# Kernel tuning notes

Hardware: AMD Instinct MI355X
Metric: run time of the kernel (lower is better)

The kernel has to match this reference:

```python
import jax, jax.numpy as jnp
import numpy as np

B, S, D, H, F, E = 2, 1024, 1024, 16, 2048, 8
HD = D // H


def _ln(x, g, b, eps=1e-5):
    m = x.mean(-1, keepdims=True)
    v = ((x - m) ** 2).mean(-1, keepdims=True)
    return (x - m) / jnp.sqrt(v + eps) * g + b


def setup_inputs() -> dict:
    key = jax.random.key(0)
    ks = jax.random.split(key, 12)
    rn = lambda k, shp, s=0.02: jax.random.normal(k, shp, jnp.float32) * s
    return {
        'src': jax.random.normal(ks[0], (B, S, D), jnp.float32),
        'q_w': rn(ks[1], (D, D)),
        'k_w': rn(ks[2], (D, D)),
        'v_w': rn(ks[3], (D, D)),
        'out_w': rn(ks[4], (D, D)),
        'gate_w': rn(ks[5], (D, D)),
        'gate_b': rn(ks[6], (D,)),
        'scale_w': rn(ks[7], (H, HD)),
        'n1_g': jnp.ones((D,), jnp.float32),
        'n1_b': jnp.zeros((D,), jnp.float32),
        'n2_g': jnp.ones((D,), jnp.float32),
        'n2_b': jnp.zeros((D,), jnp.float32),
        'moe_gate_w': rn(ks[8], (D, E)),
        'moe_gate_b': jnp.zeros((E,), jnp.float32),
        'w1': rn(ks[9], (E, D, F)),
        'b1': jnp.zeros((E, F), jnp.float32),
        'ln_g': jnp.ones((E, F), jnp.float32),
        'ln_b': jnp.zeros((E, F), jnp.float32),
        'w2': rn(ks[10], (E, F, D)),
        'b2': jnp.zeros((E, D), jnp.float32),
        'res_scale': jnp.ones((E,), jnp.float32),
    }


def reference(src, q_w, k_w, v_w, out_w, gate_w, gate_b, scale_w,
              n1_g, n1_b, n2_g, n2_b, moe_gate_w, moe_gate_b,
              w1, b1, ln_g, ln_b, w2, b2, res_scale):
    b, s, d = src.shape
    h = scale_w.shape[0]
    hd = d // h
    # --- MemoAttention (gated, dynamically scaled), eval mode ---
    q = (src @ q_w).reshape(b, s, h, hd).transpose(0, 2, 1, 3)  # [b,h,s,hd]
    k = (src @ k_w).reshape(b, s, h, hd).transpose(0, 2, 1, 3)
    v = (src @ v_w).reshape(b, s, h, hd).transpose(0, 2, 1, 3)
    scores = jnp.einsum('bhqd,bhkd->bhqk', q, k) / np.float32(np.sqrt(hd))
    scale = jax.nn.sigmoid(jnp.einsum('bhsd,hd->bhs', q, scale_w)) * 2.0
    scores = scores * scale[..., None]
    aw = jax.nn.softmax(scores, axis=-1)
    out = jnp.einsum('bhqk,bhkd->bhqd', aw, v).transpose(0, 2, 1, 3).reshape(b, s, d)
    gate = jax.nn.sigmoid(out @ gate_w + gate_b)
    attn = (out * gate) @ out_w
    # --- residual + norm1 ---
    x = _ln(src + attn, n1_g, n1_b)
    # --- MoE FFN (top-2 routing; torch loop overwrites -> last (max-index) expert
    xr = x.reshape(-1, d)                      # [N, d]
    n = xr.shape[0]
    logits = xr @ moe_gate_w + moe_gate_b       # [N, E]
    top_v, top_i = jax.lax.top_k(logits, 2)
    wts = jax.nn.softmax(top_v, axis=-1)        # [N, 2]
    chosen = jnp.max(top_i, axis=-1)            # last-written expert per token

    def expert(W1, B1, G, Bt, W2, B2, rsc):
        hh = xr @ W1 + B1                       # [N, F]
        hh = jax.nn.gelu(_ln(hh, G, Bt), approximate=False)
        return (hh @ W2 + B2) * rsc + xr        # [N, d]

    outs = jax.vmap(expert)(w1, b1, ln_g, ln_b, w2, b2, res_scale)  # [E,N,d]
    sel = jnp.take_along_axis(outs.transpose(1, 0, 2), chosen[:, None, None], axis=1)[:, 0]
    moe = sel * jnp.sum(wts, axis=-1, keepdims=True)
    # --- residual + norm2 ---
    return _ln(x + moe.reshape(b, s, d), n2_g, n2_b)
```

## Files before the change

### kernel.cpp

```cpp
#include <hip/hip_runtime.h>


typedef _Float16 f16;
typedef _Float16 f16x8 __attribute__((ext_vector_type(8)));
typedef _Float16 f16x4 __attribute__((ext_vector_type(4)));
typedef float f32x4 __attribute__((ext_vector_type(4)));

constexpr int CS  = 1024;
constexpr int CD  = 1024;
constexpr int CH  = 16;
constexpr int CHD = 64;
constexpr int CF  = 2048;
constexpr int CE  = 8;
constexpr int CN  = 2048;
constexpr int CBH = 32;
constexpr int KS  = 512;
constexpr int MAXT = 48;

constexpr float LO_SCALE = 2048.f;
constexpr float LO_INV   = 1.f / 2048.f;

#define MFMA16(a, b, c) __builtin_amdgcn_mfma_f32_16x16x32_f16((a), (b), (c), 0, 0, 0)

#define TO_GBL(p) ((const __attribute__((address_space(1))) void*)(p))
#define TO_LDS(p) ((__attribute__((address_space(3))) void*)(p))
#define GLD16(g, l) __builtin_amdgcn_global_load_lds(TO_GBL(g), TO_LDS(l), 16, 0, 0)

__device__ __forceinline__ void fsplit(float v, f16 &hi, f16 &lo) {
  hi = (f16)v;
  lo = (f16)((v - (float)hi) * LO_SCALE);
}


__global__ void k_split_cvt(const float* __restrict__ in, f16* __restrict__ oh,
                            f16* __restrict__ ol, int n) {
  int i = (blockIdx.x * blockDim.x + threadIdx.x) * 4;
  if (i >= n) return;
  float4 v = *(const float4*)(in + i);
  float a[4] = {v.x, v.y, v.z, v.w};
  f16x4 vh, vl;
#pragma unroll
  for (int j = 0; j < 4; ++j) {
    f16 hi = (f16)a[j];
    vh[j] = hi;
    vl[j] = (f16)((a[j] - (float)hi) * LO_SCALE);
  }
  *(f16x4*)(oh + i) = vh;
  *(f16x4*)(ol + i) = vl;
}

// ... 2 lines not shown
    f16* __restrict__ ol, int R, int C) {
  __shared__ float t[64][65];
  const int z = blockIdx.z;
  const float* src = in + (size_t)z * R * C;
  f16* dh = oh + (size_t)z * R * C;
  f16* dl = ol ? ol + (size_t)z * R * C : nullptr;
  const int c0 = blockIdx.x * 64, r0 = blockIdx.y * 64;
  const int tt = threadIdx.x;
  const int lane = tt & 63, wv = tt >> 6;
#pragma unroll
  for (int i = 0; i < 16; ++i)
    t[wv + i * 4][lane] = src[(size_t)(r0 + wv + i * 4) * C + c0 + lane];
  __syncthreads();
  const int oc = tt >> 4;
  const int og = tt & 15;
#pragma unroll
  for (int cc = 0; cc < 64; cc += 16) {
    f16x4 vh, vl;
#pragma unroll
    for (int j = 0; j < 4; ++j) {
      const float v = t[og * 4 + j][cc + oc];
      f16 hi = (f16)v;
      vh[j] = hi;
      vl[j] = (f16)((v - (float)hi) * LO_SCALE);
    }
    const size_t idx = (size_t)(c0 + cc + oc) * R + r0 + og * 4;
    *(f16x4*)(dh + idx) = vh;
    if (dl) *(f16x4*)(dl + idx) = vl;
  }
}


template <bool SPLIT>
__device__ __forceinline__ void gemm_tile_db(
    const f16* aH, const f16* aL, const f16* bH, const f16* bL,
    size_t bRowStride , int K, f16* lds,
    f32x4 (&accm)[2][4], f32x4 (&accc)[2][4]) {
  constexpr int BUF = SPLIT ? 12288 : 6144;
  constexpr int BOFF = SPLIT ? 4096 : 2048;
  const int t = threadIdx.x;
  const int lane = t & 63, wave = t >> 6;
  const int wm = wave >> 1, wn = wave & 1;
  const int m16 = lane & 15, quad = lane >> 4;
  int aoff[2], boff[4];
#pragma unroll
  for (int sm = 0; sm < 2; ++sm) {
    const int r = wm * 32 + sm * 16 + m16;
    aoff[sm] = r * 32 + ((quad ^ ((r >> 1) & 3)) * 8);
  }
#pragma unroll
  for (int sn = 0; sn < 4; ++sn) {
    const int r = wn * 64 + sn * 16 + m16;
    boff[sn] = BOFF + r * 32 + ((quad ^ ((r >> 1) & 3)) * 8);
  }
  auto stage = [&](f16* buf) {
    GLD16(aH, buf + t * 8);
    GLD16(bH, buf + BOFF + t * 8);
    GLD16(bH + bRowStride, buf + BOFF + 2048 + t * 8);
    if constexpr (SPLIT) {
      GLD16(aL, buf + 2048 + t * 8);
      GLD16(bL, buf + 8192 + t * 8);
      GLD16(bL + bRowStride, buf + 10240 + t * 8);
      aL += 32; bL += 32;
    }
    aH += 32; bH += 32;
  };
  stage(lds);
  stage(lds + BUF);
  int cur = 0;
  for (int k = 0; k < K; k += 32) {
    if (k + 32 < K) {
      if constexpr (SPLIT) asm volatile("s_waitcnt vmcnt(6)" ::: "memory");
      else                 asm volatile("s_waitcnt vmcnt(3)" ::: "memory");
    } else {
      asm volatile("s_waitcnt vmcnt(0)" ::: "memory");
    }
    __builtin_amdgcn_s_barrier();
    asm volatile("" ::: "memory");
    f16* buf = lds + cur * BUF;
    if (k + 64 < K) {
      int pf = cur + 2; if (pf >= 3) pf -= 3;
      stage(lds + pf * BUF);
    }
    f16x8 af[2], alf[2], bf[4], blf[4];
#pragma unroll
    for (int sm = 0; sm < 2; ++sm) {
      af[sm] = *(const f16x8*)(buf + aoff[sm]);
      if constexpr (SPLIT) alf[sm] = *(const f16x8*)(buf + 2048 + aoff[sm]);
    }
#pragma unroll
    for (int sn = 0; sn < 4; ++sn) {
      bf[sn] = *(const f16x8*)(buf + boff[sn]);
      if constexpr (SPLIT) blf[sn] = *(const f16x8*)(buf + 4096 + boff[sn]);
    }
#pragma unroll
    for (int sm = 0; sm < 2; ++sm)
#pragma unroll
      for (int sn = 0; sn < 4; ++sn) {
        accm[sm][sn] = MFMA16(af[sm], bf[sn], accm[sm][sn]);
        if constexpr (SPLIT) {
          accc[sm][sn] = MFMA16(af[sm], blf[sn], accc[sm][sn]);
          accc[sm][sn] = MFMA16(alf[sm], bf[sn], accc[sm][sn]);
        }
      }
    if (++cur == 3) cur = 0;
  }
}


__global__ __launch_bounds__(256) void g_qkv(
    const f16* __restrict__ srcH, const f16* __restrict__ srcL,
    const f16* __restrict__ qwH, const f16* __restrict__ qwL,
    const f16* __restrict__ kwH, const f16* __restrict__ kwL,
    const f16* __restrict__ vwH, const f16* __restrict__ vwL,
    f16* __restrict__ qHo, f16* __restrict__ qLo,
    f16* __restrict__ kHo, f16* __restrict__ kLo,
    f16* __restrict__ vTH, f16* __restrict__ vTL) {
  __shared__ f16 lds[36864];
  const int z = blockIdx.z;
  const int m0 = blockIdx.x * 64, n0 = blockIdx.y * 128;
  const int t = threadIdx.x;
  const int rowS = t >> 2;
  const int ksw = ((t & 3) ^ ((rowS >> 1) & 3)) * 8;
  const f16* BH = (z == 0) ? qwH : (z == 1) ? kwH : vwH;
  const f16* BL = (z == 0) ? qwL : (z == 1) ? kwL : vwL;
  const f32x4 VZ = {0.f, 0.f, 0.f, 0.f};
  f32x4 accm[2][4], accc[2][4];
#pragma unroll
  for (int i = 0; i < 2; ++i)
#pragma unroll
    for (int j = 0; j < 4; ++j) { accm[i][j] = VZ; accc[i][j] = VZ; }
  gemm_tile_db<true>(srcH + (size_t)(m0 + rowS) * CD + ksw,
                     srcL + (size_t)(m0 + rowS) * CD + ksw,
                     BH + (size_t)(n0 + rowS) * CD + ksw,
                     BL + (size_t)(n0 + rowS) * CD + ksw,
                     (size_t)64 * CD, CD, lds, accm, accc);
  const int lane = t & 63, wave = t >> 6;
  const int wm = wave >> 1, wn = wave & 1;
  const int m16 = lane & 15, quad = lane >> 4;
#pragma unroll
  for (int sm = 0; sm < 2; ++sm)
#pragma unroll
    for (int sn = 0; sn < 4; ++sn)
#pragma unroll
      for (int r = 0; r < 4; ++r) {
        const int row = m0 + wm * 32 + sm * 16 + quad * 4 + r;
        const int col = n0 + wn * 64 + sn * 16 + m16;
        const float v = accm[sm][sn][r] + accc[sm][sn][r] * LO_INV;
        f16 hi, lo; fsplit(v, hi, lo);
        const int bb = row >> 10, ss = row & 1023;
        const int hh = col >> 6, hd = col & 63;
        if (z == 2) {
          const size_t idx = ((size_t)((bb * CH + hh) * CHD + hd)) * CS + ss;
          vTH[idx] = hi; vTL[idx] = lo;
        } else {
          const size_t idx = ((size_t)((bb * CH + hh) * CS + ss)) * CHD + hd;
          if (z == 0) { qHo[idx] = hi; qLo[idx] = lo; }
          else        { kHo[idx] = hi; kLo[idx] = lo; }
        }
      }
}


__device__ __forceinline__ int pswz(int q, int k) {
  return q * 64 + ((((k >> 2) ^ q) & 15) << 2) + (k & 3);
}

__global__ __launch_bounds__(256) void k_fattn(
    const f16* __restrict__ qH_, const f16* __restrict__ qL_,
    const f16* __restrict__ kH_, const f16* __restrict__ kL_,
    const f16* __restrict__ vTH_, const f16* __restrict__ vTL_,
    const float* __restrict__ scale_w,
    f16* __restrict__ aoH, f16* __restrict__ aoL) {
  __shared__ f16 kvb[32768];
  __shared__ float psc[4 * 1024];
  const int bh = blockIdx.y;
  const int b = bh >> 4, h = bh & 15;
  const int t = threadIdx.x;
  const int lane = t & 63, wave = t >> 6;
// ... 20 lines not shown
  };

  const f16* qrh = qH_ + ((size_t)bh * CS + q0 + m16) * CHD + quad * 8;
  const f16* qrl = qL_ + ((size_t)bh * CS + q0 + m16) * CHD + quad * 8;
  f16x8 a0h = *(const f16x8*)(qrh);
  f16x8 a1h = *(const f16x8*)(qrh + 32);
  f16x8 a0l = *(const f16x8*)(qrl);
  f16x8 a1l = *(const f16x8*)(qrl + 32);

  stage(kvb, 0);

  float dot = 0.f;
  {
    const float* sw = scale_w + h * CHD + quad * 8;
    float4 s0 = *(const float4*)(sw);
    float4 s1 = *(const float4*)(sw + 4);
    float4 s2 = *(const float4*)(sw + 32);
    float4 s3 = *(const float4*)(sw + 36);
    float sv[16] = {s0.x, s0.y, s0.z, s0.w, s1.x, s1.y, s1.z, s1.w,
                    s2.x, s2.y, s2.z, s2.w, s3.x, s3.y, s3.z, s3.w};
#pragma unroll
    for (int j = 0; j < 8; ++j) {
      dot += ((float)a0h[j] + (float)a0l[j] * LO_INV) * sv[j];
      dot += ((float)a1h[j] + (float)a1l[j] * LO_INV) * sv[8 + j];
    }
    dot += __shfl_xor(dot, 16);
    dot += __shfl_xor(dot, 32);
  }
  const float qsv = 2.f / (1.f + __expf(-dot));
  float qsr[4];
#pragma unroll
  for (int r = 0; r < 4; ++r) qsr[r] = __shfl(qsv, quad * 4 + r) * 0.125f;

  f32x4 accm[4], accc[4];
#pragma unroll
  for (int tt = 0; tt < 4; ++tt) { accm[tt] = VZ; accc[tt] = VZ; }
  float mrun[4], lrun[4];
#pragma unroll
  for (int r = 0; r < 4; ++r) { mrun[r] = -1e30f; lrun[r] = 0.f; }

  int cur = 0;
  for (int kc = 0; kc < CS; kc += 64) {
    __syncthreads();
    const f16* kv = kvb + cur * 16384;
    if (kc + 64 < CS) stage(kvb + (cur ^ 1) * 16384, kc + 64);

    f32x4 st[4];
#pragma unroll
    for (int tt = 0; tt < 4; ++tt) {
      const int r = tt * 16 + m16;
      f16x8 b0h = ldf(kv,        r, quad);
      f16x8 b1h = ldf(kv,        r, quad + 4);
      f16x8 b0l = ldf(kv + 4096, r, quad);
      f16x8 b1l = ldf(kv + 4096, r, quad + 4);
      f32x4 am = VZ, ac = VZ;
      am = MFMA16(a0h, b0h, am); am = MFMA16(a1h, b1h, am);
      ac = MFMA16(a0h, b0l, ac); ac = MFMA16(a0l, b0h, ac);
      ac = MFMA16(a1h, b1l, ac); ac = MFMA16(a1l, b1h, ac);
#pragma unroll
      for (int r4 = 0; r4 < 4; ++r4)
        st[tt][r4] = (am[r4] + ac[r4] * LO_INV) * qsr[r4];
    }
    float alpha[4];
#pragma unroll
    for (int r = 0; r < 4; ++r) {
      float mx = fmaxf(fmaxf(st[0][r], st[1][r]), fmaxf(st[2][r], st[3][r]));
#pragma unroll
      for (int msk = 8; msk >= 1; msk >>= 1) mx = fmaxf(mx, __shfl_xor(mx, msk));
      const float mnew = fmaxf(mrun[r], mx);
      alpha[r] = __expf(mrun[r] - mnew);
      mrun[r] = mnew;
    }
    float rs[4] = {0.f, 0.f, 0.f, 0.f};
#pragma unroll
    for (int tt = 0; tt < 4; ++tt)
#pragma unroll
      for (int r = 0; r < 4; ++r) {
        const float e = __expf(st[tt][r] - mrun[r]);
        rs[r] += e;
        P[pswz(quad * 4 + r, tt * 16 + m16)] = e;
      }
#pragma unroll
    for (int r = 0; r < 4; ++r) {
#pragma unroll
      for (int msk = 8; msk >= 1; msk >>= 1) rs[r] += __shfl_xor(rs[r], msk);
      lrun[r] = lrun[r] * alpha[r] + rs[r];
#pragma unroll
      for (int tt = 0; tt < 4; ++tt) { accm[tt][r] *= alpha[r]; accc[tt][r] *= alpha[r]; }
    }
    f16x8 pah[2], pal[2];
#pragma unroll
    for (int c = 0; c < 2; ++c) {
      const int k0 = c * 32 + quad * 8;
      float4 p0 = *(const float4*)(P + pswz(m16, k0));
      float4 p1 = *(const float4*)(P + pswz(m16, k0 + 4));
      float pv[8] = {p0.x, p0.y, p0.z, p0.w, p1.x, p1.y, p1.z, p1.w};
#pragma unroll
      for (int j = 0; j < 8; ++j) {
        f16 hi = (f16)pv[j];
        pah[c][j] = hi;
        pal[c][j] = (f16)((pv[j] - (float)hi) * LO_SCALE);
      }
    }
#pragma unroll
    for (int tt = 0; tt < 4; ++tt) {
      const int r = tt * 16 + m16;
#pragma unroll
      for (int c = 0; c < 2; ++c) {
        f16x8 vbh = ldf(kv + 8192,  r, quad + 4 * c);
        f16x8 vbl = ldf(kv + 12288, r, quad + 4 * c);
        accm[tt] = MFMA16(pah[c], vbh, accm[tt]);
        accc[tt] = MFMA16(pah[c], vbl, accc[tt]);
        accc[tt] = MFMA16(pal[c], vbh, accc[tt]);
      }
    }
    cur ^= 1;
  }
#pragma unroll
  for (int tt = 0; tt < 4; ++tt)
#pragma unroll
    for (int r = 0; r < 4; ++r) {
      const int row = q0 + quad * 4 + r;
      const float v = (accm[tt][r] + accc[tt][r] * LO_INV) / lrun[r];
      f16 hi, lo; fsplit(v, hi, lo);
      const size_t idx = ((size_t)(b * CS + row)) * CD + h * CHD + tt * 16 + m16;
      aoH[idx] = hi; aoL[idx] = lo;
    }
}


__global__ __launch_bounds__(256) void g_gate(
    const f16* __restrict__ aoH, const f16* __restrict__ aoL,
    const f16* __restrict__ gwH, const f16* __restrict__ gwL,
    float* __restrict__ gpre ) {
  __shared__ f16 lds[36864];
  const int m0 = blockIdx.x * 64, n0 = blockIdx.y * 128, s = blockIdx.z;
  const int t = threadIdx.x;
  const int rowS = t >> 2;
  const int ksw = ((t & 3) ^ ((rowS >> 1) & 3)) * 8;
  const int k0 = s * KS;
  const f32x4 VZ = {0.f, 0.f, 0.f, 0.f};
  f32x4 accm[2][4], accc[2][4];
#pragma unroll
  for (int i = 0; i < 2; ++i)
#pragma unroll
    for (int j = 0; j < 4; ++j) { accm[i][j] = VZ; accc[i][j] = VZ; }
  gemm_tile_db<true>(aoH + (size_t)(m0 + rowS) * CD + k0 + ksw,
                     aoL + (size_t)(m0 + rowS) * CD + k0 + ksw,
                     gwH + (size_t)(n0 + rowS) * CD + k0 + ksw,
                     gwL + (size_t)(n0 + rowS) * CD + k0 + ksw,
                     (size_t)64 * CD, KS, lds, accm, accc);
  float* gp = gpre + (size_t)s * CN * CD;
  const int lane = t & 63, wave = t >> 6;
  const int wm = wave >> 1, wn = wave & 1;
  const int m16 = lane & 15, quad = lane >> 4;
#pragma unroll
  for (int sm = 0; sm < 2; ++sm)
#pragma unroll
    for (int sn = 0; sn < 4; ++sn)
#pragma unroll
      for (int r = 0; r < 4; ++r) {
        const int row = m0 + wm * 32 + sm * 16 + quad * 4 + r;
        const int col = n0 + wn * 64 + sn * 16 + m16;
        gp[(size_t)row * CD + col] = accm[sm][sn][r] + accc[sm][sn][r] * LO_INV;
      }
}

__global__ __launch_bounds__(256) void k_gatemul(
    const float* __restrict__ gpre, const f16* __restrict__ aoH,
    const f16* __restrict__ aoL, const float* __restrict__ gate_b,
    f16* __restrict__ gdH, f16* __restrict__ gdL) {
  const int i = (blockIdx.x * 256 + threadIdx.x) * 4;
  float4 p0 = *(const float4*)(gpre + i);
  float4 p1 = *(const float4*)(gpre + (size_t)CN * CD + i);
  float4 gb = *(const float4*)(gate_b + (i & (CD - 1)));
  f16x4 ah = *(const f16x4*)(aoH + i);
  f16x4 al = *(const f16x4*)(aoL + i);
  float pre[4] = {p0.x + p1.x + gb.x, p0.y + p1.y + gb.y,
                  p0.z + p1.z + gb.z, p0.w + p1.w + gb.w};
  f16x4 oh, ol;
#pragma unroll
  for (int j = 0; j < 4; ++j) {
    const float g = 1.f / (1.f + __expf(-pre[j]));
    const float ov = ((float)ah[j] + (float)al[j] * LO_INV) * g;
    f16 hi, lo; fsplit(ov, hi, lo);
    oh[j] = hi; ol[j] = lo;
  }
  *(f16x4*)(gdH + i) = oh;
  *(f16x4*)(gdL + i) = ol;
}

__global__ __launch_bounds__(256) void g_outp(
    const f16* __restrict__ gdH, const f16* __restrict__ gdL,
    const f16* __restrict__ owH, const f16* __restrict__ owL,
    float* __restrict__ y1p ) {
  __shared__ f16 lds[36864];
  const int m0 = blockIdx.x * 64, n0 = blockIdx.y * 128, s = blockIdx.z;
  const int t = threadIdx.x;
  const int rowS = t >> 2;
  const int ksw = ((t & 3) ^ ((rowS >> 1) & 3)) * 8;
  const int k0 = s * KS;
  const f32x4 VZ = {0.f, 0.f, 0.f, 0.f};
  f32x4 accm[2][4], accc[2][4];
#pragma unroll
  for (int i = 0; i < 2; ++i)
#pragma unroll
    for (int j = 0; j < 4; ++j) { accm[i][j] = VZ; accc[i][j] = VZ; }
  gemm_tile_db<true>(gdH + (size_t)(m0 + rowS) * CD + k0 + ksw,
                     gdL + (size_t)(m0 + rowS) * CD + k0 + ksw,
                     owH + (size_t)(n0 + rowS) * CD + k0 + ksw,
                     owL + (size_t)(n0 + rowS) * CD + k0 + ksw,
                     (size_t)64 * CD, KS, lds, accm, accc);
  float* yp = y1p + (size_t)s * CN * CD;
  const int lane = t & 63, wave = t >> 6;
  const int wm = wave >> 1, wn = wave & 1;
  const int m16 = lane & 15, quad = lane >> 4;
#pragma unroll
  for (int sm = 0; sm < 2; ++sm)
#pragma unroll
    for (int sn = 0; sn < 4; ++sn)
#pragma unroll
      for (int r = 0; r < 4; ++r) {
        const int row = m0 + wm * 32 + sm * 16 + quad * 4 + r;
        const int col = n0 + wn * 64 + sn * 16 + m16;
        yp[(size_t)row * CD + col] = accm[sm][sn][r] + accc[sm][sn][r] * LO_INV;
      }
}


__device__ __forceinline__ void block_reduce2(float &s, float &ss, float* red) {
#pragma unroll
  for (int msk = 32; msk >= 1; msk >>= 1) {
    s += __shfl_xor(s, msk);
    ss += __shfl_xor(ss, msk);
  }
  const int wave = threadIdx.x >> 6, lane = threadIdx.x & 63;
  if (lane == 0) { red[wave] = s; red[4 + wave] = ss; }
  __syncthreads();
  s = red[0] + red[1] + red[2] + red[3];
  ss = red[4] + red[5] + red[6] + red[7];
}

__global__ __launch_bounds__(256) void k_ln1(
    const float* __restrict__ y1p, const float* __restrict__ srcp,
    const float* __restrict__ g, const float* __restrict__ bb,
    float* __restrict__ x, f16* __restrict__ xH) {
  __shared__ float red[8];
  const int n = blockIdx.x;
  const int t = threadIdx.x;
  const size_t off = (size_t)n * CD + t * 4;
  float4 v0 = *(const float4*)(y1p + off);
  float4 v1 = *(const float4*)(y1p + (size_t)CN * CD + off);
  float4 v2 = *(const float4*)(srcp + off);
  float a[4] = {v0.x + v1.x + v2.x, v0.y + v1.y + v2.y,
                v0.z + v1.z + v2.z, v0.w + v1.w + v2.w};
  float s = a[0] + a[1] + a[2] + a[3];
// ... 63 lines not shown
  for (int j = 0; j < 16; ++j) {
    const int d = lane * 16 + j;
    const float xv = xr[d];
    const float* wr = gw + (size_t)d * CE;
#pragma unroll
    for (int e = 0; e < CE; ++e) acc[e] += xv * wr[e];
  }
#pragma unroll
  for (int msk = 32; msk >= 1; msk >>= 1) {
#pragma unroll
    for (int e = 0; e < CE; ++e) acc[e] += __shfl_xor(acc[e], msk);
  }
  if (lane == 0) {
    float best = -1e30f, second = -1e30f;
    int bi = 0, si = 0;
#pragma unroll
    for (int e = 0; e < CE; ++e) {
      const float L = acc[e] + gb[e];
      if (L > best) { second = best; si = bi; best = L; bi = e; }
      else if (L > second) { second = L; si = e; }
    }
    const int ch = bi > si ? bi : si;
    chosen[n] = ch;
    const int pos = atomicAdd(&counts[ch], 1);
    bucket[ch * CN + pos] = n;
  }
}

__global__ void k_plan(const int* __restrict__ counts, int* __restrict__ tiles) {
  if (threadIdx.x == 0) {
    int n = 0;
    for (int e = 0; e < CE; ++e) {
      const int c = counts[e];
      for (int m0 = 0; m0 < c; m0 += 64) { tiles[2 * n] = e; tiles[2 * n + 1] = m0; ++n; }
    }
    for (; n < MAXT; ++n) { tiles[2 * n] = -1; tiles[2 * n + 1] = 0; }
  }
}


__global__ __launch_bounds__(256) void g_moe1(
    const f16* __restrict__ xH, const f16* __restrict__ w1t,
    const int* __restrict__ counts, const int* __restrict__ bucket,
    const int* __restrict__ tiles, float* __restrict__ hbp ) {
  const int e = tiles[2 * blockIdx.x];
  if (e < 0) return;
  const int m0 = tiles[2 * blockIdx.x + 1];
  const int cnt = counts[e];
  const int s = blockIdx.z;
  __shared__ f16 lds[18432];
  const int t = threadIdx.x;
  const int rowS = t >> 2;
  const int ksw = ((t & 3) ^ ((rowS >> 1) & 3)) * 8;
  const int k0 = s * KS;
  int ra = m0 + rowS; if (ra > cnt - 1) ra = cnt - 1;
  const int tokA = bucket[e * CN + ra];
  const int n0 = blockIdx.y * 128;
  const f32x4 VZ = {0.f, 0.f, 0.f, 0.f};
  f32x4 accm[2][4], accd[2][4];
#pragma unroll
  for (int i = 0; i < 2; ++i)
#pragma unroll
    for (int j = 0; j < 4; ++j) { accm[i][j] = VZ; accd[i][j] = VZ; }
  gemm_tile_db<false>(xH + (size_t)tokA * CD + k0 + ksw, nullptr,
                      w1t + ((size_t)e * CF + n0 + rowS) * CD + k0 + ksw, nullptr,
                      (size_t)64 * CD, KS, lds, accm, accd);
  float* hp = hbp + (size_t)s * CN * CF;
  const int lane = t & 63, wave = t >> 6;
  const int wm = wave >> 1, wn = wave & 1;
  const int m16 = lane & 15, quad = lane >> 4;
#pragma unroll
  for (int sm = 0; sm < 2; ++sm)
#pragma unroll
    for (int sn = 0; sn < 4; ++sn)
#pragma unroll
      for (int r = 0; r < 4; ++r) {
        const int rr = m0 + wm * 32 + sm * 16 + quad * 4 + r;
        if (rr >= cnt) continue;
        const int tok = bucket[e * CN + rr];
        const int col = n0 + wn * 64 + sn * 16 + m16;
        hp[(size_t)tok * CF + col] = accm[sm][sn][r];
      }
}

__global__ __launch_bounds__(256) void k_lngelu(
    const float* __restrict__ hbp, const int* __restrict__ chosen,
    const float* __restrict__ b1,
    const float* __restrict__ ln_g, const float* __restrict__ ln_b,
    f16* __restrict__ h2) {
  __shared__ float red[8];
  const int n = blockIdx.x;
  const int e = chosen[n];
  const int t = threadIdx.x;
  const size_t off = (size_t)n * CF + t * 8;
  float4 v0 = *(const float4*)(hbp + off);
  float4 v1 = *(const float4*)(hbp + off + 4);
  float4 u0 = *(const float4*)(hbp + (size_t)CN * CF + off);
  float4 u1 = *(const float4*)(hbp + (size_t)CN * CF + off + 4);
  float4 b0 = *(const float4*)(b1 + (size_t)e * CF + t * 8);
  float4 b1v = *(const float4*)(b1 + (size_t)e * CF + t * 8 + 4);
  float a[8] = {v0.x + u0.x + b0.x, v0.y + u0.y + b0.y,
                v0.z + u0.z + b0.z, v0.w + u0.w + b0.w,
                v1.x + u1.x + b1v.x, v1.y + u1.y + b1v.y,
                v1.z + u1.z + b1v.z, v1.w + u1.w + b1v.w};
  float s = 0.f, ss = 0.f;
#pragma unroll
  for (int j = 0; j < 8; ++j) { s += a[j]; ss += a[j] * a[j]; }
  block_reduce2(s, ss, red);
  const float mean = s * (1.f / CF);
  const float var = ss * (1.f / CF) - mean * mean;
  const float rstd = rsqrtf(var + 1e-5f);
  const float* g = ln_g + (size_t)e * CF;
  const float* bb = ln_b + (size_t)e * CF;
#pragma unroll
  for (int j = 0; j < 8; ++j) {
    const int d = t * 8 + j;
    const float val = (a[j] - mean) * rstd * g[d] + bb[d];
    const float gl = 0.5f * val * (1.f + erff(val * 0.70710678118654752f));
    h2[(size_t)n * CF + d] = (f16)gl;
  }
}

__global__ __launch_bounds__(256) void g_moe2(
    const f16* __restrict__ h2, const f16* __restrict__ w2t,
    const int* __restrict__ counts, const int* __restrict__ bucket,
    const int* __restrict__ tiles, float* __restrict__ zbp ) {
  const int e = tiles[2 * blockIdx.x];
  if (e < 0) return;
  const int m0 = tiles[2 * blockIdx.x + 1];
  const int cnt = counts[e];
  const int s = blockIdx.z;
  __shared__ f16 lds[18432];
  const int t = threadIdx.x;
  const int rowS = t >> 2;
  const int ksw = ((t & 3) ^ ((rowS >> 1) & 3)) * 8;
  const int k0 = s * KS;
  int ra = m0 + rowS; if (ra > cnt - 1) ra = cnt - 1;
  const int tokA = bucket[e * CN + ra];
  const int n0 = blockIdx.y * 128;
  const f32x4 VZ = {0.f, 0.f, 0.f, 0.f};
  f32x4 accm[2][4], accd[2][4];
#pragma unroll
  for (int i = 0; i < 2; ++i)
#pragma unroll
    for (int j = 0; j < 4; ++j) { accm[i][j] = VZ; accd[i][j] = VZ; }
  gemm_tile_db<false>(h2 + (size_t)tokA * CF + k0 + ksw, nullptr,
                      w2t + ((size_t)e * CD + n0 + rowS) * CF + k0 + ksw, nullptr,
                      (size_t)64 * CF, KS, lds, accm, accd);
  float* zp = zbp + (size_t)s * CN * CD;
  const int lane = t & 63, wave = t >> 6;
  const int wm = wave >> 1, wn = wave & 1;
  const int m16 = lane & 15, quad = lane >> 4;
#pragma unroll
  for (int sm = 0; sm < 2; ++sm)
#pragma unroll
    for (int sn = 0; sn < 4; ++sn)
#pragma unroll
      for (int r = 0; r < 4; ++r) {
        const int rr = m0 + wm * 32 + sm * 16 + quad * 4 + r;
        if (rr >= cnt) continue;
        const int tok = bucket[e * CN + rr];
        const int col = n0 + wn * 64 + sn * 16 + m16;
        zp[(size_t)tok * CD + col] = accm[sm][sn][r];
      }
}


extern "C" void kernel_launch(void* const* d_in, const int* in_sizes, int n_in,
                              void* d_out, int out_size, void* d_ws, size_t ws_size,
                              hipStream_t stream) {
  (void)in_sizes; (void)n_in; (void)out_size; (void)ws_size;
  const float* src        = (const float*)d_in[0];
  const float* q_w        = (const float*)d_in[1];
  const float* k_w        = (const float*)d_in[2];
  const float* v_w        = (const float*)d_in[3];
  const float* out_w      = (const float*)d_in[4];
  const float* gate_w     = (const float*)d_in[5];
  const float* gate_b     = (const float*)d_in[6];
  const float* scale_w    = (const float*)d_in[7];
  const float* n1_g       = (const float*)d_in[8];
  const float* n1_b       = (const float*)d_in[9];
  const float* n2_g       = (const float*)d_in[10];
  const float* n2_b       = (const float*)d_in[11];
  const float* moe_gate_w = (const float*)d_in[12];
  const float* moe_gate_b = (const float*)d_in[13];
  const float* w1         = (const float*)d_in[14];
  const float* b1         = (const float*)d_in[15];
  const float* ln_g       = (const float*)d_in[16];
  const float* ln_b       = (const float*)d_in[17];
  const float* w2         = (const float*)d_in[18];
  const float* b2         = (const float*)d_in[19];
  const float* res_scale  = (const float*)d_in[20];
// ... 17 lines not shown
  f16* gwL = (f16*)take((size_t)CD * CD * 2);
  f16* owH = (f16*)take((size_t)CD * CD * 2);
  f16* owL = (f16*)take((size_t)CD * CD * 2);
  f16* qH = (f16*)take((size_t)CBH * CS * CHD * 2);
  f16* qL = (f16*)take((size_t)CBH * CS * CHD * 2);
  f16* kH = (f16*)take((size_t)CBH * CS * CHD * 2);
  f16* kL = (f16*)take((size_t)CBH * CS * CHD * 2);
  f16* vTH = (f16*)take((size_t)CBH * CS * CHD * 2);
  f16* vTL = (f16*)take((size_t)CBH * CS * CHD * 2);
  f16* aoH = (f16*)take((size_t)CN * CD * 2);
  f16* aoL = (f16*)take((size_t)CN * CD * 2);
  f16* gdH = (f16*)take((size_t)CN * CD * 2);
  f16* gdL = (f16*)take((size_t)CN * CD * 2);
  float* x  = (float*)take((size_t)CN * CD * 4);
  f16* xH = (f16*)take((size_t)CN * CD * 2);
  int* counts = (int*)take(64);
  int* bucket = (int*)take((size_t)CE * CN * 4);
  int* chosen = (int*)take((size_t)CN * 4);
  int* tiles = (int*)take((size_t)MAXT * 2 * 4);
  f16* h2 = (f16*)take((size_t)CN * CF * 2);
  f16* w1t = (f16*)take((size_t)CE * CF * CD * 2);
  f16* w2t = (f16*)take((size_t)CE * CD * CF * 2);
  float* pbuf = (float*)take((size_t)4 * CN * CD * 4);

  k_split_cvt<<<dim3(CN * CD / 4 / 256), 256, 0, stream>>>(src, srcH, srcL, CN * CD);
  k_transpose_split<<<dim3(CD / 64, CD / 64, 1), 256, 0, stream>>>(q_w, qwH, qwL, CD, CD);
  k_transpose_split<<<dim3(CD / 64, CD / 64, 1), 256, 0, stream>>>(k_w, kwH, kwL, CD, CD);
  k_transpose_split<<<dim3(CD / 64, CD / 64, 1), 256, 0, stream>>>(v_w, vwH, vwL, CD, CD);
  k_transpose_split<<<dim3(CD / 64, CD / 64, 1), 256, 0, stream>>>(gate_w, gwH, gwL, CD, CD);
  k_transpose_split<<<dim3(CD / 64, CD / 64, 1), 256, 0, stream>>>(out_w, owH, owL, CD, CD);
  k_transpose_split<<<dim3(CF / 64, CD / 64, CE), 256, 0, stream>>>(w1, w1t, nullptr, CD, CF);
  k_transpose_split<<<dim3(CD / 64, CF / 64, CE), 256, 0, stream>>>(w2, w2t, nullptr, CF, CD);

  g_qkv<<<dim3(CN / 64, CD / 128, 3), 256, 0, stream>>>(
      srcH, srcL, qwH, qwL, kwH, kwL, vwH, vwL, qH, qL, kH, kL, vTH, vTL);
  k_fattn<<<dim3(CS / 64, CBH), 256, 0, stream>>>(
      qH, qL, kH, kL, vTH, vTL, scale_w, aoH, aoL);
  g_gate<<<dim3(CN / 64, CD / 128, 2), 256, 0, stream>>>(aoH, aoL, gwH, gwL, pbuf);
  k_gatemul<<<dim3(CN * CD / 4 / 256), 256, 0, stream>>>(pbuf, aoH, aoL, gate_b, gdH, gdL);
  g_outp<<<dim3(CN / 64, CD / 128, 2), 256, 0, stream>>>(gdH, gdL, owH, owL, pbuf);
  k_ln1<<<dim3(CN), 256, 0, stream>>>(pbuf, src, n1_g, n1_b, x, xH);

  k_zero_counts<<<dim3(1), 64, 0, stream>>>(counts);
  k_route<<<dim3(CN / 4), 256, 0, stream>>>(x, moe_gate_w, moe_gate_b, chosen, counts, bucket);
  k_plan<<<dim3(1), 64, 0, stream>>>(counts, tiles);
  g_moe1<<<dim3(40, CF / 128, 2), 256, 0, stream>>>(xH, w1t, counts, bucket, tiles, pbuf);
  k_lngelu<<<dim3(CN), 256, 0, stream>>>(pbuf, chosen, b1, ln_g, ln_b, h2);
  g_moe2<<<dim3(40, CD / 128, 4), 256, 0, stream>>>(h2, w2t, counts, bucket, tiles, pbuf);
  k_ln2<<<dim3(CN), 256, 0, stream>>>(pbuf, x, b2, res_scale, chosen, n2_g, n2_b, outp);
}
```

Baseline: 533.7 us.

## Enlarge GEMM tiles to 128x128 with double buffering and split attention accumulators

```diff
diff --git a/kernel.cpp b/kernel.cpp
--- a/kernel.cpp
+++ b/kernel.cpp
@@ -15,7 +15,7 @@
 constexpr int CN  = 2048;
 constexpr int CBH = 32;
 constexpr int KS  = 512;
-constexpr int MAXT = 48;
+constexpr int MAXT = 24;
 
 constexpr float LO_SCALE = 2048.f;
 constexpr float LO_INV   = 1.f / 2048.f;
@@ -84,83 +84,72 @@
 
 
 template <bool SPLIT>
-__device__ __forceinline__ void gemm_tile_db(
-    const f16* aH, const f16* aL, const f16* bH, const f16* bL,
-    size_t bRowStride , int K, f16* lds,
-    f32x4 (&accm)[2][4], f32x4 (&accc)[2][4]) {
-  constexpr int BUF = SPLIT ? 12288 : 6144;
-  constexpr int BOFF = SPLIT ? 4096 : 2048;
+__device__ __forceinline__ void gemm_tile128(
+    const f16* a0, const f16* a1, const f16* al0, const f16* al1,
+    const f16* b0, const f16* b1, const f16* bl0, const f16* bl1,
+    int K, f16* lds, f32x4 (&accm)[4][4], f32x4 (&accc)[4][4]) {
+  constexpr int BUF = SPLIT ? 16384 : 8192;
+  constexpr int BO  = SPLIT ? 8192 : 4096;
   const int t = threadIdx.x;
   const int lane = t & 63, wave = t >> 6;
   const int wm = wave >> 1, wn = wave & 1;
   const int m16 = lane & 15, quad = lane >> 4;
-  int aoff[2], boff[4];
-#pragma unroll
-  for (int sm = 0; sm < 2; ++sm) {
-    const int r = wm * 32 + sm * 16 + m16;
-    aoff[sm] = r * 32 + ((quad ^ ((r >> 1) & 3)) * 8);
-  }
-#pragma unroll
-  for (int sn = 0; sn < 4; ++sn) {
-    const int r = wn * 64 + sn * 16 + m16;
-    boff[sn] = BOFF + r * 32 + ((quad ^ ((r >> 1) & 3)) * 8);
+  int aoff[4], boff[4];
+#pragma unroll
+  for (int s = 0; s < 4; ++s) {
+    const int ra = wm * 64 + s * 16 + m16;
+    aoff[s] = ra * 32 + ((quad ^ ((ra >> 1) & 3)) * 8);
+    const int rb = wn * 64 + s * 16 + m16;
+    boff[s] = BO + rb * 32 + ((quad ^ ((rb >> 1) & 3)) * 8);
   }
   auto stage = [&](f16* buf) {
-    GLD16(aH, buf + t * 8);
-    GLD16(bH, buf + BOFF + t * 8);
-    GLD16(bH + bRowStride, buf + BOFF + 2048 + t * 8);
+    GLD16(a0, buf + t * 8);
+    GLD16(a1, buf + 2048 + t * 8);
+    GLD16(b0, buf + BO + t * 8);
+    GLD16(b1, buf + BO + 2048 + t * 8);
     if constexpr (SPLIT) {
-      GLD16(aL, buf + 2048 + t * 8);
-      GLD16(bL, buf + 8192 + t * 8);
-      GLD16(bL + bRowStride, buf + 10240 + t * 8);
-      aL += 32; bL += 32;
-    }
-    aH += 32; bH += 32;
+      GLD16(al0, buf + 4096 + t * 8);
+      GLD16(al1, buf + 6144 + t * 8);
+      GLD16(bl0, buf + 12288 + t * 8);
+      GLD16(bl1, buf + 14336 + t * 8);
+      al0 += 32; al1 += 32; bl0 += 32; bl1 += 32;
+    }
+    a0 += 32; a1 += 32; b0 += 32; b1 += 32;
   };
   stage(lds);
-  stage(lds + BUF);
   int cur = 0;
   for (int k = 0; k < K; k += 32) {
-    if (k + 32 < K) {
-      if constexpr (SPLIT) asm volatile("s_waitcnt vmcnt(6)" ::: "memory");
-      else                 asm volatile("s_waitcnt vmcnt(3)" ::: "memory");
-    } else {
-      asm volatile("s_waitcnt vmcnt(0)" ::: "memory");
-    }
-    __builtin_amdgcn_s_barrier();
-    asm volatile("" ::: "memory");
+    __syncthreads();
     f16* buf = lds + cur * BUF;
-    if (k + 64 < K) {
-      int pf = cur + 2; if (pf >= 3) pf -= 3;
-      stage(lds + pf * BUF);
-    }
-    f16x8 af[2], alf[2], bf[4], blf[4];
-#pragma unroll
-    for (int sm = 0; sm < 2; ++sm) {
-      af[sm] = *(const f16x8*)(buf + aoff[sm]);
-      if constexpr (SPLIT) alf[sm] = *(const f16x8*)(buf + 2048 + aoff[sm]);
+    if (k + 32 < K) stage(lds + (cur ^ 1) * BUF);
+    f16x8 af[4], alf[4];
+#pragma unroll
+    for (int s = 0; s < 4; ++s) {
+      af[s] = *(const f16x8*)(buf + aoff[s]);
+      if constexpr (SPLIT) alf[s] = *(const f16x8*)(buf + 4096 + aoff[s]);
     }
 #pragma unroll
     for (int sn = 0; sn < 4; ++sn) {
-      bf[sn] = *(const f16x8*)(buf + boff[sn]);
-      if constexpr (SPLIT) blf[sn] = *(const f16x8*)(buf + 4096 + boff[sn]);
-    }
-#pragma unroll
-    for (int sm = 0; sm < 2; ++sm)
-#pragma unroll
-      for (int sn = 0; sn < 4; ++sn) {
-        accm[sm][sn] = MFMA16(af[sm], bf[sn], accm[sm][sn]);
-        if constexpr (SPLIT) {
-          accc[sm][sn] = MFMA16(af[sm], blf[sn], accc[sm][sn]);
-          accc[sm][sn] = MFMA16(alf[sm], bf[sn], accc[sm][sn]);
-        }
-      }
-    if (++cur == 3) cur = 0;
-  }
-}
-
-
-__global__ __launch_bounds__(256) void g_qkv(
+      const f16x8 bf = *(const f16x8*)(buf + boff[sn]);
+#pragma unroll
+      for (int sm = 0; sm < 4; ++sm)
+        accm[sm][sn] = MFMA16(af[sm], bf, accm[sm][sn]);
+      if constexpr (SPLIT) {
+        const f16x8 blf = *(const f16x8*)(buf + 4096 + boff[sn]);
+#pragma unroll
+        for (int sm = 0; sm < 4; ++sm)
+          accc[sm][sn] = MFMA16(af[sm], blf, accc[sm][sn]);
+#pragma unroll
+        for (int sm = 0; sm < 4; ++sm)
+          accc[sm][sn] = MFMA16(alf[sm], bf, accc[sm][sn]);
+      }
+    }
+    cur ^= 1;
+  }
+}
+
+
+__global__ __launch_bounds__(256, 2) void g_qkv(
     const f16* __restrict__ srcH, const f16* __restrict__ srcL,
     const f16* __restrict__ qwH, const f16* __restrict__ qwL,
     const f16* __restrict__ kwH, const f16* __restrict__ kwL,
@@ -168,35 +157,37 @@
     f16* __restrict__ qHo, f16* __restrict__ qLo,
     f16* __restrict__ kHo, f16* __restrict__ kLo,
     f16* __restrict__ vTH, f16* __restrict__ vTL) {
-  __shared__ f16 lds[36864];
+  __shared__ f16 lds[32768];
   const int z = blockIdx.z;
-  const int m0 = blockIdx.x * 64, n0 = blockIdx.y * 128;
+  const int m0 = blockIdx.x * 128, n0 = blockIdx.y * 128;
   const int t = threadIdx.x;
   const int rowS = t >> 2;
   const int ksw = ((t & 3) ^ ((rowS >> 1) & 3)) * 8;
   const f16* BH = (z == 0) ? qwH : (z == 1) ? kwH : vwH;
   const f16* BL = (z == 0) ? qwL : (z == 1) ? kwL : vwL;
+  const f16* A0 = srcH + (size_t)(m0 + rowS) * CD + ksw;
+  const f16* AL0 = srcL + (size_t)(m0 + rowS) * CD + ksw;
+  const f16* B0 = BH + (size_t)(n0 + rowS) * CD + ksw;
+  const f16* BL0 = BL + (size_t)(n0 + rowS) * CD + ksw;
   const f32x4 VZ = {0.f, 0.f, 0.f, 0.f};
-  f32x4 accm[2][4], accc[2][4];
-#pragma unroll
-  for (int i = 0; i < 2; ++i)
+  f32x4 accm[4][4], accc[4][4];
+#pragma unroll
+  for (int i = 0; i < 4; ++i)
 #pragma unroll
     for (int j = 0; j < 4; ++j) { accm[i][j] = VZ; accc[i][j] = VZ; }
-  gemm_tile_db<true>(srcH + (size_t)(m0 + rowS) * CD + ksw,
-                     srcL + (size_t)(m0 + rowS) * CD + ksw,
-                     BH + (size_t)(n0 + rowS) * CD + ksw,
-                     BL + (size_t)(n0 + rowS) * CD + ksw,
-                     (size_t)64 * CD, CD, lds, accm, accc);
+  gemm_tile128<true>(A0, A0 + (size_t)64 * CD, AL0, AL0 + (size_t)64 * CD,
+                     B0, B0 + (size_t)64 * CD, BL0, BL0 + (size_t)64 * CD,
+                     CD, lds, accm, accc);
   const int lane = t & 63, wave = t >> 6;
   const int wm = wave >> 1, wn = wave & 1;
   const int m16 = lane & 15, quad = lane >> 4;
 #pragma unroll
-  for (int sm = 0; sm < 2; ++sm)
+  for (int sm = 0; sm < 4; ++sm)
 #pragma unroll
     for (int sn = 0; sn < 4; ++sn)
 #pragma unroll
       for (int r = 0; r < 4; ++r) {
-        const int row = m0 + wm * 32 + sm * 16 + quad * 4 + r;
+        const int row = m0 + wm * 64 + sm * 16 + quad * 4 + r;
         const int col = n0 + wn * 64 + sn * 16 + m16;
         const float v = accm[sm][sn][r] + accc[sm][sn][r] * LO_INV;
         f16 hi, lo; fsplit(v, hi, lo);
@@ -283,9 +274,9 @@
 #pragma unroll
   for (int r = 0; r < 4; ++r) qsr[r] = __shfl(qsv, quad * 4 + r) * 0.125f;
 
-  f32x4 accm[4], accc[4];
-#pragma unroll
-  for (int tt = 0; tt < 4; ++tt) { accm[tt] = VZ; accc[tt] = VZ; }
+  f32x4 accm[4], accc[4], accd[4];
+#pragma unroll
+  for (int tt = 0; tt < 4; ++tt) { accm[tt] = VZ; accc[tt] = VZ; accd[tt] = VZ; }
   float mrun[4], lrun[4];
 #pragma unroll
   for (int r = 0; r < 4; ++r) { mrun[r] = -1e30f; lrun[r] = 0.f; }
@@ -304,13 +295,13 @@
       f16x8 b1h = ldf(kv,        r, quad + 4);
       f16x8 b0l = ldf(kv + 4096, r, quad);
       f16x8 b1l = ldf(kv + 4096, r, quad + 4);
-      f32x4 am = VZ, ac = VZ;
+      f32x4 am = VZ, ac1 = VZ, ac2 = VZ;
       am = MFMA16(a0h, b0h, am); am = MFMA16(a1h, b1h, am);
-      ac = MFMA16(a0h, b0l, ac); ac = MFMA16(a0l, b0h, ac);
-      ac = MFMA16(a1h, b1l, ac); ac = MFMA16(a1l, b1h, ac);
+      ac1 = MFMA16(a0h, b0l, ac1); ac2 = MFMA16(a0l, b0h, ac2);
+      ac1 = MFMA16(a1h, b1l, ac1); ac2 = MFMA16(a1l, b1h, ac2);
 #pragma unroll
       for (int r4 = 0; r4 < 4; ++r4)
-        st[tt][r4] = (am[r4] + ac[r4] * LO_INV) * qsr[r4];
+        st[tt][r4] = (am[r4] + (ac1[r4] + ac2[r4]) * LO_INV) * qsr[r4];
     }
     float alpha[4];
 #pragma unroll
@@ -337,7 +328,9 @@
       for (int msk = 8; msk >= 1; msk >>= 1) rs[r] += __shfl_xor(rs[r], msk);
       lrun[r] = lrun[r] * alpha[r] + rs[r];
 #pragma unroll
-      for (int tt = 0; tt < 4; ++tt) { accm[tt][r] *= alpha[r]; accc[tt][r] *= alpha[r]; }
+      for (int tt = 0; tt < 4; ++tt) {
+        accm[tt][r] *= alpha[r]; accc[tt][r] *= alpha[r]; accd[tt][r] *= alpha[r];
+      }
     }
     f16x8 pah[2], pal[2];
 #pragma unroll
@@ -354,17 +347,16 @@
       }
     }
 #pragma unroll
-    for (int tt = 0; tt < 4; ++tt) {
-      const int r = tt * 16 + m16;
-#pragma unroll
-      for (int c = 0; c < 2; ++c) {
+    for (int c = 0; c < 2; ++c)
+#pragma unroll
+      for (int tt = 0; tt < 4; ++tt) {
+        const int r = tt * 16 + m16;
         f16x8 vbh = ldf(kv + 8192,  r, quad + 4 * c);
         f16x8 vbl = ldf(kv + 12288, r, quad + 4 * c);
         accm[tt] = MFMA16(pah[c], vbh, accm[tt]);
         accc[tt] = MFMA16(pah[c], vbl, accc[tt]);
-        accc[tt] = MFMA16(pal[c], vbh, accc[tt]);
-      }
-    }
+        accd[tt] = MFMA16(pal[c], vbh, accd[tt]);
+      }
     cur ^= 1;
   }
 #pragma unroll
@@ -372,7 +364,8 @@
 #pragma unroll
     for (int r = 0; r < 4; ++r) {
       const int row = q0 + quad * 4 + r;
-      const float v = (accm[tt][r] + accc[tt][r] * LO_INV) / lrun[r];
+      const float v =
+          (accm[tt][r] + (accc[tt][r] + accd[tt][r]) * LO_INV) / lrun[r];
       f16 hi, lo; fsplit(v, hi, lo);
       const size_t idx = ((size_t)(b * CS + row)) * CD + h * CHD + tt * 16 + m16;
       aoH[idx] = hi; aoL[idx] = lo;
@@ -380,38 +373,40 @@
 }
 
 
-__global__ __launch_bounds__(256) void g_gate(
+__global__ __launch_bounds__(256, 2) void g_gate(
     const f16* __restrict__ aoH, const f16* __restrict__ aoL,
     const f16* __restrict__ gwH, const f16* __restrict__ gwL,
     float* __restrict__ gpre ) {
-  __shared__ f16 lds[36864];
-  const int m0 = blockIdx.x * 64, n0 = blockIdx.y * 128, s = blockIdx.z;
+  __shared__ f16 lds[32768];
+  const int m0 = blockIdx.x * 128, n0 = blockIdx.y * 128, s = blockIdx.z;
   const int t = threadIdx.x;
   const int rowS = t >> 2;
   const int ksw = ((t & 3) ^ ((rowS >> 1) & 3)) * 8;
   const int k0 = s * KS;
+  const f16* A0 = aoH + (size_t)(m0 + rowS) * CD + k0 + ksw;
+  const f16* AL0 = aoL + (size_t)(m0 + rowS) * CD + k0 + ksw;
+  const f16* B0 = gwH + (size_t)(n0 + rowS) * CD + k0 + ksw;
+  const f16* BL0 = gwL + (size_t)(n0 + rowS) * CD + k0 + ksw;
   const f32x4 VZ = {0.f, 0.f, 0.f, 0.f};
-  f32x4 accm[2][4], accc[2][4];
-#pragma unroll
-  for (int i = 0; i < 2; ++i)
+  f32x4 accm[4][4], accc[4][4];
+#pragma unroll
+  for (int i = 0; i < 4; ++i)
 #pragma unroll
     for (int j = 0; j < 4; ++j) { accm[i][j] = VZ; accc[i][j] = VZ; }
-  gemm_tile_db<true>(aoH + (size_t)(m0 + rowS) * CD + k0 + ksw,
-                     aoL + (size_t)(m0 + rowS) * CD + k0 + ksw,
-                     gwH + (size_t)(n0 + rowS) * CD + k0 + ksw,
-                     gwL + (size_t)(n0 + rowS) * CD + k0 + ksw,
-                     (size_t)64 * CD, KS, lds, accm, accc);
+  gemm_tile128<true>(A0, A0 + (size_t)64 * CD, AL0, AL0 + (size_t)64 * CD,
+                     B0, B0 + (size_t)64 * CD, BL0, BL0 + (size_t)64 * CD,
+                     KS, lds, accm, accc);
   float* gp = gpre + (size_t)s * CN * CD;
   const int lane = t & 63, wave = t >> 6;
   const int wm = wave >> 1, wn = wave & 1;
   const int m16 = lane & 15, quad = lane >> 4;
 #pragma unroll
-  for (int sm = 0; sm < 2; ++sm)
+  for (int sm = 0; sm < 4; ++sm)
 #pragma unroll
     for (int sn = 0; sn < 4; ++sn)
 #pragma unroll
       for (int r = 0; r < 4; ++r) {
-        const int row = m0 + wm * 32 + sm * 16 + quad * 4 + r;
+        const int row = m0 + wm * 64 + sm * 16 + quad * 4 + r;
         const int col = n0 + wn * 64 + sn * 16 + m16;
         gp[(size_t)row * CD + col] = accm[sm][sn][r] + accc[sm][sn][r] * LO_INV;
       }
@@ -441,38 +436,40 @@
   *(f16x4*)(gdL + i) = ol;
 }
 
-__global__ __launch_bounds__(256) void g_outp(
+__global__ __launch_bounds__(256, 2) void g_outp(
     const f16* __restrict__ gdH, const f16* __restrict__ gdL,
     const f16* __restrict__ owH, const f16* __restrict__ owL,
     float* __restrict__ y1p ) {
-  __shared__ f16 lds[36864];
-  const int m0 = blockIdx.x * 64, n0 = blockIdx.y * 128, s = blockIdx.z;
+  __shared__ f16 lds[32768];
+  const int m0 = blockIdx.x * 128, n0 = blockIdx.y * 128, s = blockIdx.z;
   const int t = threadIdx.x;
   const int rowS = t >> 2;
   const int ksw = ((t & 3) ^ ((rowS >> 1) & 3)) * 8;
   const int k0 = s * KS;
+  const f16* A0 = gdH + (size_t)(m0 + rowS) * CD + k0 + ksw;
+  const f16* AL0 = gdL + (size_t)(m0 + rowS) * CD + k0 + ksw;
+  const f16* B0 = owH + (size_t)(n0 + rowS) * CD + k0 + ksw;
+  const f16* BL0 = owL + (size_t)(n0 + rowS) * CD + k0 + ksw;
   const f32x4 VZ = {0.f, 0.f, 0.f, 0.f};
-  f32x4 accm[2][4], accc[2][4];
-#pragma unroll
-  for (int i = 0; i < 2; ++i)
+  f32x4 accm[4][4], accc[4][4];
+#pragma unroll
+  for (int i = 0; i < 4; ++i)
 #pragma unroll
     for (int j = 0; j < 4; ++j) { accm[i][j] = VZ; accc[i][j] = VZ; }
-  gemm_tile_db<true>(gdH + (size_t)(m0 + rowS) * CD + k0 + ksw,
-                     gdL + (size_t)(m0 + rowS) * CD + k0 + ksw,
-                     owH + (size_t)(n0 + rowS) * CD + k0 + ksw,
-                     owL + (size_t)(n0 + rowS) * CD + k0 + ksw,
-                     (size_t)64 * CD, KS, lds, accm, accc);
+  gemm_tile128<true>(A0, A0 + (size_t)64 * CD, AL0, AL0 + (size_t)64 * CD,
+                     B0, B0 + (size_t)64 * CD, BL0, BL0 + (size_t)64 * CD,
+                     KS, lds, accm, accc);
   float* yp = y1p + (size_t)s * CN * CD;
   const int lane = t & 63, wave = t >> 6;
   const int wm = wave >> 1, wn = wave & 1;
   const int m16 = lane & 15, quad = lane >> 4;
 #pragma unroll
-  for (int sm = 0; sm < 2; ++sm)
+  for (int sm = 0; sm < 4; ++sm)
 #pragma unroll
     for (int sn = 0; sn < 4; ++sn)
 #pragma unroll
       for (int r = 0; r < 4; ++r) {
-        const int row = m0 + wm * 32 + sm * 16 + quad * 4 + r;
+        const int row = m0 + wm * 64 + sm * 16 + quad * 4 + r;
         const int col = n0 + wn * 64 + sn * 16 + m16;
         yp[(size_t)row * CD + col] = accm[sm][sn][r] + accc[sm][sn][r] * LO_INV;
       }
@@ -602,14 +599,14 @@
     int n = 0;
     for (int e = 0; e < CE; ++e) {
       const int c = counts[e];
-      for (int m0 = 0; m0 < c; m0 += 64) { tiles[2 * n] = e; tiles[2 * n + 1] = m0; ++n; }
+      for (int m0 = 0; m0 < c; m0 += 128) { tiles[2 * n] = e; tiles[2 * n + 1] = m0; ++n; }
     }
     for (; n < MAXT; ++n) { tiles[2 * n] = -1; tiles[2 * n + 1] = 0; }
   }
 }
 
 
-__global__ __launch_bounds__(256) void g_moe1(
+__global__ __launch_bounds__(256, 2) void g_moe1(
     const f16* __restrict__ xH, const f16* __restrict__ w1t,
     const int* __restrict__ counts, const int* __restrict__ bucket,
     const int* __restrict__ tiles, float* __restrict__ hbp ) {
@@ -618,34 +615,38 @@
   const int m0 = tiles[2 * blockIdx.x + 1];
   const int cnt = counts[e];
   const int s = blockIdx.z;
-  __shared__ f16 lds[18432];
+  __shared__ f16 lds[16384];
   const int t = threadIdx.x;
   const int rowS = t >> 2;
   const int ksw = ((t & 3) ^ ((rowS >> 1) & 3)) * 8;
   const int k0 = s * KS;
-  int ra = m0 + rowS; if (ra > cnt - 1) ra = cnt - 1;
-  const int tokA = bucket[e * CN + ra];
+  int ra0 = m0 + rowS;      if (ra0 > cnt - 1) ra0 = cnt - 1;
+  int ra1 = m0 + rowS + 64; if (ra1 > cnt - 1) ra1 = cnt - 1;
+  const int tok0 = bucket[e * CN + ra0];
+  const int tok1 = bucket[e * CN + ra1];
   const int n0 = blockIdx.y * 128;
+  const f16* B0 = w1t + ((size_t)e * CF + n0 + rowS) * CD + k0 + ksw;
   const f32x4 VZ = {0.f, 0.f, 0.f, 0.f};
-  f32x4 accm[2][4], accd[2][4];
-#pragma unroll
-  for (int i = 0; i < 2; ++i)
+  f32x4 accm[4][4], accd[4][4];
+#pragma unroll
+  for (int i = 0; i < 4; ++i)
 #pragma unroll
     for (int j = 0; j < 4; ++j) { accm[i][j] = VZ; accd[i][j] = VZ; }
-  gemm_tile_db<false>(xH + (size_t)tokA * CD + k0 + ksw, nullptr,
-                      w1t + ((size_t)e * CF + n0 + rowS) * CD + k0 + ksw, nullptr,
-                      (size_t)64 * CD, KS, lds, accm, accd);
+  gemm_tile128<false>(xH + (size_t)tok0 * CD + k0 + ksw,
+                      xH + (size_t)tok1 * CD + k0 + ksw, nullptr, nullptr,
+                      B0, B0 + (size_t)64 * CD, nullptr, nullptr,
+                      KS, lds, accm, accd);
   float* hp = hbp + (size_t)s * CN * CF;
   const int lane = t & 63, wave = t >> 6;
   const int wm = wave >> 1, wn = wave & 1;
   const int m16 = lane & 15, quad = lane >> 4;
 #pragma unroll
-  for (int sm = 0; sm < 2; ++sm)
+  for (int sm = 0; sm < 4; ++sm)
 #pragma unroll
     for (int sn = 0; sn < 4; ++sn)
 #pragma unroll
       for (int r = 0; r < 4; ++r) {
-        const int rr = m0 + wm * 32 + sm * 16 + quad * 4 + r;
+        const int rr = m0 + wm * 64 + sm * 16 + quad * 4 + r;
         if (rr >= cnt) continue;
         const int tok = bucket[e * CN + rr];
         const int col = n0 + wn * 64 + sn * 16 + m16;
@@ -691,7 +692,7 @@
   }
 }
 
-__global__ __launch_bounds__(256) void g_moe2(
+__global__ __launch_bounds__(256, 2) void g_moe2(
     const f16* __restrict__ h2, const f16* __restrict__ w2t,
     const int* __restrict__ counts, const int* __restrict__ bucket,
     const int* __restrict__ tiles, float* __restrict__ zbp ) {
@@ -700,34 +701,38 @@
   const int m0 = tiles[2 * blockIdx.x + 1];
   const int cnt = counts[e];
   const int s = blockIdx.z;
-  __shared__ f16 lds[18432];
+  __shared__ f16 lds[16384];
   const int t = threadIdx.x;
   const int rowS = t >> 2;
   const int ksw = ((t & 3) ^ ((rowS >> 1) & 3)) * 8;
   const int k0 = s * KS;
-  int ra = m0 + rowS; if (ra > cnt - 1) ra = cnt - 1;
-  const int tokA = bucket[e * CN + ra];
+  int ra0 = m0 + rowS;      if (ra0 > cnt - 1) ra0 = cnt - 1;
+  int ra1 = m0 + rowS + 64; if (ra1 > cnt - 1) ra1 = cnt - 1;
+  const int tok0 = bucket[e * CN + ra0];
+  const int tok1 = bucket[e * CN + ra1];
   const int n0 = blockIdx.y * 128;
+  const f16* B0 = w2t + ((size_t)e * CD + n0 + rowS) * CF + k0 + ksw;
   const f32x4 VZ = {0.f, 0.f, 0.f, 0.f};
-  f32x4 accm[2][4], accd[2][4];
-#pragma unroll
-  for (int i = 0; i < 2; ++i)
+  f32x4 accm[4][4], accd[4][4];
+#pragma unroll
+  for (int i = 0; i < 4; ++i)
 #pragma unroll
     for (int j = 0; j < 4; ++j) { accm[i][j] = VZ; accd[i][j] = VZ; }
-  gemm_tile_db<false>(h2 + (size_t)tokA * CF + k0 + ksw, nullptr,
-                      w2t + ((size_t)e * CD + n0 + rowS) * CF + k0 + ksw, nullptr,
-                      (size_t)64 * CF, KS, lds, accm, accd);
+  gemm_tile128<false>(h2 + (size_t)tok0 * CF + k0 + ksw,
+                      h2 + (size_t)tok1 * CF + k0 + ksw, nullptr, nullptr,
+                      B0, B0 + (size_t)64 * CF, nullptr, nullptr,
+                      KS, lds, accm, accd);
   float* zp = zbp + (size_t)s * CN * CD;
   const int lane = t & 63, wave = t >> 6;
   const int wm = wave >> 1, wn = wave & 1;
   const int m16 = lane & 15, quad = lane >> 4;
 #pragma unroll
-  for (int sm = 0; sm < 2; ++sm)
+  for (int sm = 0; sm < 4; ++sm)
 #pragma unroll
     for (int sn = 0; sn < 4; ++sn)
 #pragma unroll
       for (int r = 0; r < 4; ++r) {
-        const int rr = m0 + wm * 32 + sm * 16 + quad * 4 + r;
+        const int rr = m0 + wm * 64 + sm * 16 + quad * 4 + r;
         if (rr >= cnt) continue;
         const int tok = bucket[e * CN + rr];
         const int col = n0 + wn * 64 + sn * 16 + m16;
@@ -811,20 +816,20 @@
   k_transpose_split<<<dim3(CF / 64, CD / 64, CE), 256, 0, stream>>>(w1, w1t, nullptr, CD, CF);
   k_transpose_split<<<dim3(CD / 64, CF / 64, CE), 256, 0, stream>>>(w2, w2t, nullptr, CF, CD);
 
-  g_qkv<<<dim3(CN / 64, CD / 128, 3), 256, 0, stream>>>(
+  g_qkv<<<dim3(CN / 128, CD / 128, 3), 256, 0, stream>>>(
       srcH, srcL, qwH, qwL, kwH, kwL, vwH, vwL, qH, qL, kH, kL, vTH, vTL);
   k_fattn<<<dim3(CS / 64, CBH), 256, 0, stream>>>(
       qH, qL, kH, kL, vTH, vTL, scale_w, aoH, aoL);
-  g_gate<<<dim3(CN / 64, CD / 128, 2), 256, 0, stream>>>(aoH, aoL, gwH, gwL, pbuf);
+  g_gate<<<dim3(CN / 128, CD / 128, 2), 256, 0, stream>>>(aoH, aoL, gwH, gwL, pbuf);
   k_gatemul<<<dim3(CN * CD / 4 / 256), 256, 0, stream>>>(pbuf, aoH, aoL, gate_b, gdH, gdL);
-  g_outp<<<dim3(CN / 64, CD / 128, 2), 256, 0, stream>>>(gdH, gdL, owH, owL, pbuf);
+  g_outp<<<dim3(CN / 128, CD / 128, 2), 256, 0, stream>>>(gdH, gdL, owH, owL, pbuf);
   k_ln1<<<dim3(CN), 256, 0, stream>>>(pbuf, src, n1_g, n1_b, x, xH);
 
   k_zero_counts<<<dim3(1), 64, 0, stream>>>(counts);
   k_route<<<dim3(CN / 4), 256, 0, stream>>>(x, moe_gate_w, moe_gate_b, chosen, counts, bucket);
   k_plan<<<dim3(1), 64, 0, stream>>>(counts, tiles);
-  g_moe1<<<dim3(40, CF / 128, 2), 256, 0, stream>>>(xH, w1t, counts, bucket, tiles, pbuf);
+  g_moe1<<<dim3(MAXT, CF / 128, 2), 256, 0, stream>>>(xH, w1t, counts, bucket, tiles, pbuf);
   k_lngelu<<<dim3(CN), 256, 0, stream>>>(pbuf, chosen, b1, ln_g, ln_b, h2);
-  g_moe2<<<dim3(40, CD / 128, 4), 256, 0, stream>>>(h2, w2t, counts, bucket, tiles, pbuf);
+  g_moe2<<<dim3(MAXT, CD / 128, 4), 256, 0, stream>>>(h2, w2t, counts, bucket, tiles, pbuf);
   k_ln2<<<dim3(CN), 256, 0, stream>>>(pbuf, x, b2, res_scale, chosen, n2_g, n2_b, outp);
 }
```

Result: faster. 515.5 us (-3.4%).
